# Kernel optimization log

Measured on AMD Instinct MI355X. Metric: run time of the kernel, lower is better.

## Reference

```python
import jax, jax.numpy as jnp
import numpy as np

N_NODES = 50000
N_EDGES = 800000
IN_SIZE = 128
NUM_HEADS = 8
HEAD_DIM = IN_SIZE // NUM_HEADS  # qk/val head dim = 16


def setup_inputs() -> dict:
    key = jax.random.key(0)
    ks = jax.random.split(key, 16)
    d = IN_SIZE
    lim = 1.0 / np.sqrt(d)
    inp = {
        "in_feats": jax.random.normal(ks[0], (N_NODES, d), jnp.float32),
        "struc_feats": jax.random.normal(ks[1], (N_NODES, d), jnp.float32),
        "edge_weights": jax.random.uniform(ks[2], (N_EDGES,), jnp.float32),
        "ln_scale": jnp.ones((d,), jnp.float32),
        "ln_bias": jnp.zeros((d,), jnp.float32),
        "Ws": jax.random.uniform(ks[3], (d, d), jnp.float32, -lim, lim),
        "bs": jnp.zeros((d,), jnp.float32),
        "Wq": jax.random.uniform(ks[4], (d, d), jnp.float32, -lim, lim),
        "bq": jnp.zeros((d,), jnp.float32),
        "Wk": jax.random.uniform(ks[5], (d, d), jnp.float32, -lim, lim),
        "bk": jnp.zeros((d,), jnp.float32),
        "Wv": jax.random.uniform(ks[6], (d, d), jnp.float32, -lim, lim),
        "bv": jnp.zeros((d,), jnp.float32),
        "Wo": jax.random.uniform(ks[7], (d, d), jnp.float32, -lim, lim),
        "edge_ids": jax.random.randint(ks[8], (2, N_EDGES), 0, N_NODES, jnp.int64)
        if jax.config.jax_enable_x64 else jax.random.randint(ks[8], (2, N_EDGES), 0, N_NODES, jnp.int32),
    }
    return inp


def _layer_norm(x, scale, bias, eps=1e-5):
    mu = jnp.mean(x, axis=-1, keepdims=True)
    var = jnp.var(x, axis=-1, keepdims=True)
    return (x - mu) * jax.lax.rsqrt(var + eps) * scale + bias


def reference(in_feats, struc_feats, edge_weights, ln_scale, ln_bias,
              Ws, bs, Wq, bq, Wk, bk, Wv, bv, Wo, edge_ids):
    N = in_feats.shape[0]
    H, hd = NUM_HEADS, HEAD_DIM

    delta = _layer_norm(in_feats, ln_scale, ln_bias)           # pre-norm
    delta = jax.nn.gelu(delta, approximate=False)               # pre-activation (exact GELU, torch default)
    delta_struc = delta + struc_feats @ Ws.T + bs               # struc_proj add

    qry = (delta_struc @ Wq.T + bq) / np.sqrt(hd)                # [N, qk]
    keyf = delta_struc @ Wk.T + bk                               # [N, qk]
    val = delta @ Wv.T + bv                                      # [N, val]

    src, dst = edge_ids[0], edge_ids[1]                          # out[src] += A[src,dst] * val[dst]
    qe = qry[src].reshape(-1, H, hd)                             # [E, H, hd]
    ke = keyf[dst].reshape(-1, H, hd)                            # [E, H, hd]
    attn = jax.nn.sigmoid(jnp.sum(qe * ke, axis=-1))             # [E, H]
    attn = edge_weights[:, None] * attn

    msgs = attn[:, :, None] * val[dst].reshape(-1, H, hd)        # [E, H, hd]
    agg = jax.ops.segment_sum(msgs.reshape(-1, H * hd), src, num_segments=N)  # [N, val]

    out = agg @ Wo.T                                             # out_proj (no bias)
    return in_feats + out                                        # skip connection
```

## Files before the change

### kernel.cpp

```cpp
#include <hip/hip_runtime.h>
#include <math.h>

#define NF 128

typedef __attribute__((ext_vector_type(8))) short short8;
typedef __attribute__((ext_vector_type(4))) float floatx4;

__device__ __forceinline__ unsigned short f2bf(float f) {
    union { float x; unsigned int i; } c; c.x = f;
    unsigned int r = c.i + 0x7fffu + ((c.i >> 16) & 1u);
    return (unsigned short)(r >> 16);
}
__device__ __forceinline__ float bf2f(unsigned short u) {
    union { unsigned int i; float x; } c; c.i = ((unsigned int)u) << 16;
    return c.x;
}
__device__ __forceinline__ void unpack8(uint4 u, float* f) {
    union { unsigned int i; float x; } c;
    c.i = u.x << 16;          f[0] = c.x;
    c.i = u.x & 0xffff0000u;  f[1] = c.x;
    c.i = u.y << 16;          f[2] = c.x;
    c.i = u.y & 0xffff0000u;  f[3] = c.x;
    c.i = u.z << 16;          f[4] = c.x;
    c.i = u.z & 0xffff0000u;  f[5] = c.x;
    c.i = u.w << 16;          f[6] = c.x;
    c.i = u.w & 0xffff0000u;  f[7] = c.x;
}
__device__ __forceinline__ ushort4 pack4(float a, float b, float c, float d) {
    ushort4 h; h.x = f2bf(a); h.y = f2bf(b); h.z = f2bf(c); h.w = f2bf(d);
    return h;
}

__global__ __launch_bounds__(256) void wconv5_kernel(
    const float* __restrict__ a, const float* __restrict__ b,
    const float* __restrict__ c, const float* __restrict__ d,
    const float* __restrict__ e, unsigned short* __restrict__ o)
{
    int i = blockIdx.x * 256 + threadIdx.x;
    int w = i >> 14, j = i & 16383;
    const float* p = (w == 0) ? a : (w == 1) ? b : (w == 2) ? c : (w == 3) ? d : e;
    o[i] = f2bf(p[j]);
}

__global__ __launch_bounds__(256) void node_a_kernel(
    const float* __restrict__ in_feats, const float* __restrict__ struc,
    const float* __restrict__ gamma, const float* __restrict__ beta,
    const unsigned short* __restrict__ Wsb, const float* __restrict__ bs,
    unsigned short* __restrict__ deltab, unsigned short* __restrict__ dstrb,
    int M, int nt)
{
    __shared__ unsigned short Wl[128][136];
    __shared__ unsigned short Xs2[64][136];

    int tid = threadIdx.x;
    int lane = tid & 63, w = tid >> 6, lg = lane & 15, quad = lane >> 4;
    int lrow = tid >> 2, t4 = tid & 3;

    {
        const uint4* g = (const uint4*)Wsb;
        #pragma unroll
        for (int p = 0; p < 8; ++p) {
            int idx = tid + p * 256;
            *(uint4*)&Wl[idx >> 4][(idx & 15) * 8] = g[idx];
        }
    }
    float bsr[8];
    #pragma unroll
    for (int t = 0; t < 8; ++t) bsr[t] = bs[t * 16 + lg];
    __syncthreads();

    for (int tile = blockIdx.x; tile < nt; tile += gridDim.x) {
        int m0 = tile * 64;
        int gm = m0 + lrow;
        bool vr = gm < M;
        size_t rbase = (size_t)(vr ? gm : 0) * NF;

        uint dreg[16];
        {
            const float4* ip = (const float4*)(in_feats + rbase) + t4 * 8;
            float4 xf[8];
            #pragma unroll
            for (int p = 0; p < 8; ++p) xf[p] = ip[p];
            float s = 0.f, sq = 0.f;
            #pragma unroll
            for (int p = 0; p < 8; ++p) {
                s  += xf[p].x + xf[p].y + xf[p].z + xf[p].w;
                sq += xf[p].x * xf[p].x + xf[p].y * xf[p].y
                    + xf[p].z * xf[p].z + xf[p].w * xf[p].w;
            }
            s  += __shfl_xor(s, 1, 64);  s  += __shfl_xor(s, 2, 64);
            sq += __shfl_xor(sq, 1, 64); sq += __shfl_xor(sq, 2, 64);
            float mu = s * (1.0f / 128.0f);
            float var = sq * (1.0f / 128.0f) - mu * mu;
            float rstd = rsqrtf(var + 1e-5f);
            const float4* gp = (const float4*)gamma + t4 * 8;
            const float4* bp = (const float4*)beta + t4 * 8;
            #pragma unroll
            for (int p = 0; p < 8; ++p) {
                float4 g4 = gp[p], b4 = bp[p];
                float o0 = (xf[p].x - mu) * rstd * g4.x + b4.x;
                float o1 = (xf[p].y - mu) * rstd * g4.y + b4.y;
                float o2 = (xf[p].z - mu) * rstd * g4.z + b4.z;
                float o3 = (xf[p].w - mu) * rstd * g4.w + b4.w;
                o0 = 0.5f * o0 * (1.0f + erff(o0 * 0.70710678118654752f));
                o1 = 0.5f * o1 * (1.0f + erff(o1 * 0.70710678118654752f));
                o2 = 0.5f * o2 * (1.0f + erff(o2 * 0.70710678118654752f));
                o3 = 0.5f * o3 * (1.0f + erff(o3 * 0.70710678118654752f));
                ushort4 h = pack4(o0, o1, o2, o3);
                dreg[p * 2]     = (uint)h.x | ((uint)h.y << 16);
                dreg[p * 2 + 1] = (uint)h.z | ((uint)h.w << 16);
            }
            if (vr) {
                uint4* od = (uint4*)(deltab + (size_t)gm * NF + t4 * 32);
                #pragma unroll
                for (int q = 0; q < 4; ++q)
                    od[q] = make_uint4(dreg[q*4], dreg[q*4+1], dreg[q*4+2], dreg[q*4+3]);
            }
            const float4* sp = (const float4*)(struc + rbase) + t4 * 8;
            #pragma unroll
            for (int p = 0; p < 8; ++p) {
                float4 f = sp[p];
                *(ushort4*)&Xs2[lrow][t4 * 32 + p * 4] = pack4(f.x, f.y, f.z, f.w);
            }
        }

        floatx4 acc[8];
        #pragma unroll
        for (int t = 0; t < 8; ++t) acc[t] = (floatx4){0.f, 0.f, 0.f, 0.f};
        #pragma unroll
        for (int ks = 0; ks < 4; ++ks) {
            short8 a = *(const short8*)&Xs2[w * 16 + lg][ks * 32 + quad * 8];
            #pragma unroll
            for (int t = 0; t < 8; ++t) {
                short8 b = *(const short8*)&Wl[t * 16 + lg][ks * 32 + quad * 8];
                acc[t] = __builtin_amdgcn_mfma_f32_16x16x32_bf16(a, b, acc[t], 0, 0, 0);
            }
        }

        #pragma unroll
        for (int q = 0; q < 4; ++q)
            *(uint4*)&Xs2[lrow][t4 * 32 + q * 8] =
                make_uint4(dreg[q*4], dreg[q*4+1], dreg[q*4+2], dreg[q*4+3]);

        #pragma unroll
        for (int t = 0; t < 8; ++t) {
            int col = t * 16 + lg;
            #pragma unroll
            for (int r = 0; r < 4; ++r) {
                int rl = w * 16 + quad * 4 + r;
                Xs2[rl][col] = f2bf(acc[t][r] + bsr[t] + bf2f(Xs2[rl][col]));
            }
        }
        #pragma unroll
        for (int p = 0; p < 4; ++p) {
            int idx = lane + p * 64;
            int row = w * 16 + (idx >> 4), c16 = idx & 15;
            int gmo = m0 + row;
            if (gmo < M)
                *(uint4*)(dstrb + (size_t)gmo * NF + c16 * 8) = *(const uint4*)&Xs2[row][c16 * 8];
        }
    }
}

__global__ __launch_bounds__(256) void node_qkv_kernel(
    const unsigned short* __restrict__ deltab, const unsigned short* __restrict__ dstrb,
    const unsigned short* __restrict__ Wall, const float* __restrict__ bq,
    const float* __restrict__ bk, const float* __restrict__ bv,
    unsigned short* __restrict__ qb, unsigned short* __restrict__ kvb,
    int M, int nt)
{
    __shared__ unsigned short Wl[128][136];
    __shared__ unsigned short Cst[64][136];

    int tid = threadIdx.x;
    int y = blockIdx.y;
    int lane = tid & 63, w = tid >> 6, lg = lane & 15, quad = lane >> 4;

    const unsigned short* Xg = (y == 2) ? deltab : dstrb;
    const unsigned short* Wg = Wall + (y + 1) * 16384;
    const float* bias = (y == 0) ? bq : (y == 1) ? bk : bv;
    float scale = (y == 0) ? 0.25f : 1.0f;
    unsigned short* outg = (y == 0) ? qb : (y == 1) ? kvb : (kvb + NF);
    int ostride = (y == 0) ? NF : 2 * NF;

    {
        const uint4* g = (const uint4*)Wg;
        #pragma unroll
        for (int p = 0; p < 8; ++p) {
            int idx = tid + p * 256;
            *(uint4*)&Wl[idx >> 4][(idx & 15) * 8] = g[idx];
        }
    }
    float br[8];
    #pragma unroll
    for (int t = 0; t < 8; ++t) br[t] = bias[t * 16 + lg] * scale;
    __syncthreads();

    for (int tile = blockIdx.x; tile < nt; tile += gridDim.x) {
        int m0 = tile * 64;
        int am = m0 + w * 16 + lg;
        const unsigned short* arow = Xg + (size_t)(am < M ? am : 0) * NF + quad * 8;

        floatx4 acc[8];
        #pragma unroll
        for (int t = 0; t < 8; ++t) acc[t] = (floatx4){0.f, 0.f, 0.f, 0.f};
        short8 af[4];
        #pragma unroll
        for (int ks = 0; ks < 4; ++ks) af[ks] = *(const short8*)(arow + ks * 32);
        #pragma unroll
        for (int ks = 0; ks < 4; ++ks) {
            #pragma unroll
            for (int t = 0; t < 8; ++t) {
                short8 b = *(const short8*)&Wl[t * 16 + lg][ks * 32 + quad * 8];
                acc[t] = __builtin_amdgcn_mfma_f32_16x16x32_bf16(af[ks], b, acc[t], 0, 0, 0);
            }
        }
        #pragma unroll
        for (int t = 0; t < 8; ++t) {
            int col = t * 16 + lg;
            #pragma unroll
            for (int r = 0; r < 4; ++r)
                Cst[w * 16 + quad * 4 + r][col] = f2bf(acc[t][r] * scale + br[t]);
        }
        #pragma unroll
        for (int p = 0; p < 4; ++p) {
            int idx = lane + p * 64;
            int row = w * 16 + (idx >> 4), c16 = idx & 15;
            int gm = m0 + row;
            if (gm < M)
                *(uint4*)(outg + (size_t)gm * ostride + c16 * 8) = *(const uint4*)&Cst[row][c16 * 8];
        }
    }
}

__global__ __launch_bounds__(256) void gemm_out_kernel(
    const unsigned short* __restrict__ Xb, const unsigned short* __restrict__ Wb,
    const float* __restrict__ addf, float* __restrict__ Y, int M, int nt)
{
    __shared__ unsigned short Wl[128][136];
    int tid = threadIdx.x;
    int lane = tid & 63, w = tid >> 6, lg = lane & 15, quad = lane >> 4;

    {
        const uint4* g = (const uint4*)Wb;
        #pragma unroll
        for (int p = 0; p < 8; ++p) {
            int idx = tid + p * 256;
            *(uint4*)&Wl[idx >> 4][(idx & 15) * 8] = g[idx];
        }
    }
    __syncthreads();

    for (int tile = blockIdx.x; tile < nt; tile += gridDim.x) {
        int m0 = tile * 64;
        int am = m0 + w * 16 + lg;
        const unsigned short* arow = Xb + (size_t)(am < M ? am : 0) * NF + quad * 8;

        floatx4 acc[8];
        #pragma unroll
        for (int t = 0; t < 8; ++t) acc[t] = (floatx4){0.f, 0.f, 0.f, 0.f};
        short8 af[4];
        #pragma unroll
        for (int ks = 0; ks < 4; ++ks) af[ks] = *(const short8*)(arow + ks * 32);
        #pragma unroll
        for (int ks = 0; ks < 4; ++ks) {
            #pragma unroll
            for (int t = 0; t < 8; ++t) {
                short8 b = *(const short8*)&Wl[t * 16 + lg][ks * 32 + quad * 8];
                acc[t] = __builtin_amdgcn_mfma_f32_16x16x32_bf16(af[ks], b, acc[t], 0, 0, 0);
            }
        }
        #pragma unroll
        for (int t = 0; t < 8; ++t) {
            int col = t * 16 + lg;
            #pragma unroll
            for (int r = 0; r < 4; ++r) {
                int gm = m0 + w * 16 + quad * 4 + r;
                if (gm >= M) continue;
                size_t off = (size_t)gm * NF + col;
                Y[off] = acc[t][r] + addf[off];
            }
        }
    }
}

__global__ void hist_kernel(const int* __restrict__ eid, int* __restrict__ cnt, int E)
{
    int i = blockIdx.x * blockDim.x + threadIdx.x;
    if (i < E) atomicAdd(&cnt[eid[i]], 1);
}

__global__ __launch_bounds__(256) void scan1_kernel(
    const int* __restrict__ cnt, int* __restrict__ bsum, int n)
{
    int base = blockIdx.x * 1024;
    int s = 0;
    #pragma unroll
    for (int p = 0; p < 4; ++p) {
        int i = base + (int)threadIdx.x + p * 256;
        if (i < n) s += cnt[i];
    }
    #pragma unroll
    for (int m = 1; m <= 32; m <<= 1) s += __shfl_xor(s, m, 64);
    __shared__ int ws_[4];
    int wid = threadIdx.x >> 6;
    if ((threadIdx.x & 63) == 0) ws_[wid] = s;
    __syncthreads();
    if (threadIdx.x == 0) bsum[blockIdx.x] = ws_[0] + ws_[1] + ws_[2] + ws_[3];
}

__global__ __launch_bounds__(256) void scan3_kernel(
    const int* __restrict__ cnt, const int* __restrict__ bsum,
    int* __restrict__ row_start, int* __restrict__ cursor, int n, int nb)
{
    __shared__ int base_off;
    int tid = threadIdx.x, lane = tid & 63, wid = tid >> 6;
    if (tid == 0) {
        int a = 0;
        for (int j = 0; j < (int)blockIdx.x; ++j) a += bsum[j];
        base_off = a;
        if ((int)blockIdx.x == nb - 1) {
            int tot = a;
            for (int j = blockIdx.x; j < nb; ++j) tot += bsum[j];
            row_start[n] = tot;
        }
    }
    int base = blockIdx.x * 1024;
    int v[4]; int s = 0;
    #pragma unroll
    for (int p = 0; p < 4; ++p) {
        int i = base + tid * 4 + p;
        v[p] = (i < n) ? cnt[i] : 0;
        s += v[p];
    }
    int ss = s;
    #pragma unroll
    for (int off = 1; off < 64; off <<= 1) {
        int t = __shfl_up(ss, off, 64);
        if (lane >= off) ss += t;
    }
    __shared__ int wsum[4];
    if (lane == 63) wsum[wid] = ss;
    __syncthreads();
    int woff = 0;
    for (int j = 0; j < wid; ++j) woff += wsum[j];
    int a = base_off + woff + (ss - s);
    #pragma unroll
    for (int p = 0; p < 4; ++p) {
        int i = base + tid * 4 + p;
        if (i < n) { row_start[i] = a; cursor[i] = a; a += v[p]; }
    }
}

__global__ void scatter_kernel(const int* __restrict__ eid, const float* __restrict__ ew,
                               int* __restrict__ cursor, int2* __restrict__ edata, int E)
{
    int i = blockIdx.x * blockDim.x + threadIdx.x;
    if (i < E) {
        int src = eid[i];
        int dst = eid[E + i];
        int pos = atomicAdd(&cursor[src], 1);
        edata[pos] = make_int2(dst, __float_as_int(ew[i]));
    }
}

__global__ __launch_bounds__(256) void aggregate_kernel(
    const unsigned short* __restrict__ Q, const unsigned short* __restrict__ kvb,
    const int* __restrict__ row_start, const int2* __restrict__ edata,
    unsigned short* __restrict__ agg, int N)
{
    int node = blockIdx.x * 4 + (threadIdx.x >> 6);
    if (node >= N) return;
    int lane = threadIdx.x & 63;
    int sg = lane >> 4, lg = lane & 15;
    int rs = row_start[node], re = row_start[node + 1];

    float qv[8];
    unpack8(*(const uint4*)(Q + (size_t)node * NF + lg * 8), qv);
    float acc[8];
    #pragma unroll
    for (int j = 0; j < 8; ++j) acc[j] = 0.f;

    int e1 = rs + sg, e2 = rs + sg + 4;
    int2 ed1 = (e1 < re) ? edata[e1] : make_int2(0, 0);
    int2 ed2 = (e2 < re) ? edata[e2] : make_int2(0, 0);

    for (int e0 = rs; e0 < re; e0 += 8) {
        int2 c1 = ed1, c2 = ed2;
        int en1 = e0 + 8 + sg, en2 = en1 + 4;
        ed1 = (en1 < re) ? edata[en1] : make_int2(0, 0);
        ed2 = (en2 < re) ? edata[en2] : make_int2(0, 0);

        const uint4* p1 = (const uint4*)kvb + (size_t)c1.x * 32 + lg;
        const uint4* p2 = (const uint4*)kvb + (size_t)c2.x * 32 + lg;
        uint4 k1u = p1[0], v1u = p1[16];
        uint4 k2u = p2[0], v2u = p2[16];

        float kv1[8], kv2[8];
        unpack8(k1u, kv1);
        unpack8(k2u, kv2);
        float s1 = qv[0] * kv1[0], s2 = qv[0] * kv2[0];
        #pragma unroll
        for (int j = 1; j < 8; ++j) {
            s1 = fmaf(qv[j], kv1[j], s1);
            s2 = fmaf(qv[j], kv2[j], s2);
        }
        s1 += __shfl_xor(s1, 1, 64);
        s2 += __shfl_xor(s2, 1, 64);
        float a1 = __int_as_float(c1.y) / (1.f + __expf(-s1));
        float a2 = __int_as_float(c2.y) / (1.f + __expf(-s2));

        float vv1[8], vv2[8];
        unpack8(v1u, vv1);
        unpack8(v2u, vv2);
        #pragma unroll
        for (int j = 0; j < 8; ++j) {
            acc[j] = fmaf(a1, vv1[j], acc[j]);
            acc[j] = fmaf(a2, vv2[j], acc[j]);
        }
    }
    #pragma unroll
    for (int j = 0; j < 8; ++j) {
        acc[j] += __shfl_xor(acc[j], 16, 64);
        acc[j] += __shfl_xor(acc[j], 32, 64);
    }
    if (sg == 0) {
        unsigned short* o = agg + (size_t)node * NF + lg * 8;
        *(ushort4*)o       = pack4(acc[0], acc[1], acc[2], acc[3]);
        *(ushort4*)(o + 4) = pack4(acc[4], acc[5], acc[6], acc[7]);
    }
}

extern "C" void kernel_launch(void* const* d_in, const int* in_sizes, int n_in,
                              void* d_out, int out_size, void* d_ws, size_t ws_size,
                              hipStream_t stream)
{
    const float* in_feats = (const float*)d_in[0];
    const float* struc    = (const float*)d_in[1];
    const float* eweights = (const float*)d_in[2];
    const float* ln_scale = (const float*)d_in[3];
    const float* ln_bias  = (const float*)d_in[4];
    const float* Ws       = (const float*)d_in[5];
    const float* bs       = (const float*)d_in[6];
    const float* Wq       = (const float*)d_in[7];
    const float* bq       = (const float*)d_in[8];
    const float* Wk       = (const float*)d_in[9];
    const float* bk       = (const float*)d_in[10];
    const float* Wv       = (const float*)d_in[11];
    const float* bv       = (const float*)d_in[12];
    const float* Wo       = (const float*)d_in[13];
    const int*   edge_ids = (const int*)d_in[14];
    float* out = (float*)d_out;

    int N = in_sizes[0] / NF;
    int E = in_sizes[2];

    size_t F = (size_t)N * NF;
    unsigned short* deltab = (unsigned short*)d_ws;
    unsigned short* dstrb  = deltab + F;
    unsigned short* qb     = dstrb + F;
    unsigned short* kvb    = qb + F;
    unsigned short* aggb   = kvb + 2 * F;
    unsigned short* Wall   = aggb + F;
    int2*  edata     = (int2*)(Wall + 5 * 16384);
    int*   cnt       = (int*)(edata + E);
    int*   row_start = cnt + N;
    int*   cursor    = row_start + N + 1;
    int*   bsum      = cursor + N;

    int nt  = (N + 63) / 64;
    int geb = (E + 255) / 256;
    int nb  = (N + 1023) / 1024;

    wconv5_kernel<<<(5 * 16384) / 256, 256, 0, stream>>>(Ws, Wq, Wk, Wv, Wo, Wall);

    hipMemsetAsync(cnt, 0, (size_t)N * sizeof(int), stream);
    hist_kernel<<<geb, 256, 0, stream>>>(edge_ids, cnt, E);
    scan1_kernel<<<nb, 256, 0, stream>>>(cnt, bsum, N);
    scan3_kernel<<<nb, 256, 0, stream>>>(cnt, bsum, row_start, cursor, N, nb);
    scatter_kernel<<<geb, 256, 0, stream>>>(edge_ids, eweights, cursor, edata, E);

    node_a_kernel<<<392, 256, 0, stream>>>(in_feats, struc, ln_scale, ln_bias,
                                           Wall, bs, deltab, dstrb, N, nt);
    node_qkv_kernel<<<dim3(261, 3), 256, 0, stream>>>(deltab, dstrb, Wall,
                                                      bq, bk, bv, qb, kvb, N, nt);

    aggregate_kernel<<<(N + 3) / 4, 256, 0, stream>>>(qb, kvb, row_start, edata, aggb, N);

    gemm_out_kernel<<<392, 256, 0, stream>>>(aggb, Wall + 4 * 16384, in_feats, out, N, nt);
}
```

Measured before the change: 327.7 us.

## Fuse count zeroing into weight conversion, deepen aggregate prefetch, resize node grids

```diff
diff --git a/kernel.cpp b/kernel.cpp
--- a/kernel.cpp
+++ b/kernel.cpp
@@ -31,15 +31,22 @@
     return h;
 }
 
-__global__ __launch_bounds__(256) void wconv5_kernel(
+__global__ __launch_bounds__(256) void wconv5z_kernel(
     const float* __restrict__ a, const float* __restrict__ b,
     const float* __restrict__ c, const float* __restrict__ d,
-    const float* __restrict__ e, unsigned short* __restrict__ o)
-{
-    int i = blockIdx.x * 256 + threadIdx.x;
-    int w = i >> 14, j = i & 16383;
-    const float* p = (w == 0) ? a : (w == 1) ? b : (w == 2) ? c : (w == 3) ? d : e;
-    o[i] = f2bf(p[j]);
+    const float* __restrict__ e, unsigned short* __restrict__ o,
+    int* __restrict__ cnt, int N)
+{
+    int blk = blockIdx.x;
+    if (blk < 320) {
+        int i = blk * 256 + threadIdx.x;
+        int w = i >> 14, j = i & 16383;
+        const float* p = (w == 0) ? a : (w == 1) ? b : (w == 2) ? c : (w == 3) ? d : e;
+        o[i] = f2bf(p[j]);
+    } else {
+        int i = (blk - 320) * 256 + threadIdx.x;
+        if (i < N) cnt[i] = 0;
+    }
 }
 
 __global__ __launch_bounds__(256) void node_a_kernel(
@@ -381,43 +388,54 @@
     #pragma unroll
     for (int j = 0; j < 8; ++j) acc[j] = 0.f;
 
+    const uint4* kv32 = (const uint4*)kvb;
+
     int e1 = rs + sg, e2 = rs + sg + 4;
-    int2 ed1 = (e1 < re) ? edata[e1] : make_int2(0, 0);
-    int2 ed2 = (e2 < re) ? edata[e2] : make_int2(0, 0);
+    int2 edc1 = (e1     < re) ? edata[e1]     : make_int2(0, 0);
+    int2 edc2 = (e2     < re) ? edata[e2]     : make_int2(0, 0);
+    int2 edn1 = (e1 + 8 < re) ? edata[e1 + 8] : make_int2(0, 0);
+    int2 edn2 = (e2 + 8 < re) ? edata[e2 + 8] : make_int2(0, 0);
+
+    const uint4* pc1 = kv32 + (size_t)edc1.x * 32 + lg;
+    const uint4* pc2 = kv32 + (size_t)edc2.x * 32 + lg;
+    uint4 kc1 = pc1[0], vc1 = pc1[16];
+    uint4 kc2 = pc2[0], vc2 = pc2[16];
 
     for (int e0 = rs; e0 < re; e0 += 8) {
-        int2 c1 = ed1, c2 = ed2;
-        int en1 = e0 + 8 + sg, en2 = en1 + 4;
-        ed1 = (en1 < re) ? edata[en1] : make_int2(0, 0);
-        ed2 = (en2 < re) ? edata[en2] : make_int2(0, 0);
-
-        const uint4* p1 = (const uint4*)kvb + (size_t)c1.x * 32 + lg;
-        const uint4* p2 = (const uint4*)kvb + (size_t)c2.x * 32 + lg;
-        uint4 k1u = p1[0], v1u = p1[16];
-        uint4 k2u = p2[0], v2u = p2[16];
-
-        float kv1[8], kv2[8];
-        unpack8(k1u, kv1);
-        unpack8(k2u, kv2);
-        float s1 = qv[0] * kv1[0], s2 = qv[0] * kv2[0];
+        const uint4* pn1 = kv32 + (size_t)edn1.x * 32 + lg;
+        const uint4* pn2 = kv32 + (size_t)edn2.x * 32 + lg;
+        uint4 kn1 = pn1[0], vn1 = pn1[16];
+        uint4 kn2 = pn2[0], vn2 = pn2[16];
+        int f1 = e0 + 16 + sg, f2 = f1 + 4;
+        int2 edf1 = (f1 < re) ? edata[f1] : make_int2(0, 0);
+        int2 edf2 = (f2 < re) ? edata[f2] : make_int2(0, 0);
+
+        float kf1[8], kf2[8];
+        unpack8(kc1, kf1);
+        unpack8(kc2, kf2);
+        float s1 = qv[0] * kf1[0], s2 = qv[0] * kf2[0];
         #pragma unroll
         for (int j = 1; j < 8; ++j) {
-            s1 = fmaf(qv[j], kv1[j], s1);
-            s2 = fmaf(qv[j], kv2[j], s2);
+            s1 = fmaf(qv[j], kf1[j], s1);
+            s2 = fmaf(qv[j], kf2[j], s2);
         }
         s1 += __shfl_xor(s1, 1, 64);
         s2 += __shfl_xor(s2, 1, 64);
-        float a1 = __int_as_float(c1.y) / (1.f + __expf(-s1));
-        float a2 = __int_as_float(c2.y) / (1.f + __expf(-s2));
-
-        float vv1[8], vv2[8];
-        unpack8(v1u, vv1);
-        unpack8(v2u, vv2);
+        float a1 = __int_as_float(edc1.y) / (1.f + __expf(-s1));
+        float a2 = __int_as_float(edc2.y) / (1.f + __expf(-s2));
+
+        float vf1[8], vf2[8];
+        unpack8(vc1, vf1);
+        unpack8(vc2, vf2);
         #pragma unroll
         for (int j = 0; j < 8; ++j) {
-            acc[j] = fmaf(a1, vv1[j], acc[j]);
-            acc[j] = fmaf(a2, vv2[j], acc[j]);
-        }
+            acc[j] = fmaf(a1, vf1[j], acc[j]);
+            acc[j] = fmaf(a2, vf2[j], acc[j]);
+        }
+
+        kc1 = kn1; vc1 = vn1; kc2 = kn2; vc2 = vn2;
+        edc1 = edn1; edc2 = edn2;
+        edn1 = edf1; edn2 = edf2;
     }
     #pragma unroll
     for (int j = 0; j < 8; ++j) {
@@ -471,21 +489,21 @@
     int nt  = (N + 63) / 64;
     int geb = (E + 255) / 256;
     int nb  = (N + 1023) / 1024;
-
-    wconv5_kernel<<<(5 * 16384) / 256, 256, 0, stream>>>(Ws, Wq, Wk, Wv, Wo, Wall);
-
-    hipMemsetAsync(cnt, 0, (size_t)N * sizeof(int), stream);
+    int zb  = (N + 255) / 256;
+
+    wconv5z_kernel<<<320 + zb, 256, 0, stream>>>(Ws, Wq, Wk, Wv, Wo, Wall, cnt, N);
+
     hist_kernel<<<geb, 256, 0, stream>>>(edge_ids, cnt, E);
     scan1_kernel<<<nb, 256, 0, stream>>>(cnt, bsum, N);
     scan3_kernel<<<nb, 256, 0, stream>>>(cnt, bsum, row_start, cursor, N, nb);
     scatter_kernel<<<geb, 256, 0, stream>>>(edge_ids, eweights, cursor, edata, E);
 
-    node_a_kernel<<<392, 256, 0, stream>>>(in_feats, struc, ln_scale, ln_bias,
-                                           Wall, bs, deltab, dstrb, N, nt);
+    node_a_kernel<<<nt, 256, 0, stream>>>(in_feats, struc, ln_scale, ln_bias,
+                                          Wall, bs, deltab, dstrb, N, nt);
     node_qkv_kernel<<<dim3(261, 3), 256, 0, stream>>>(deltab, dstrb, Wall,
                                                       bq, bk, bv, qb, kvb, N, nt);
 
     aggregate_kernel<<<(N + 3) / 4, 256, 0, stream>>>(qb, kvb, row_start, edata, aggb, N);
 
-    gemm_out_kernel<<<392, 256, 0, stream>>>(aggb, Wall + 4 * 16384, in_feats, out, N, nt);
-}
+    gemm_out_kernel<<<nt, 256, 0, stream>>>(aggb, Wall + 4 * 16384, in_feats, out, N, nt);
+}
```

After: 323.1 us. No clear change (-1.4%).
